# Kernel optimization log

Measured on AMD Instinct MI355X. Metric: run time of the kernel, lower is better.

Reference implementation:

```python
import jax, jax.numpy as jnp
import numpy as np

B, N, D, F, H, C, L = 64, 8192, 5, 16, 4, 4, 4
NEG_SLOPE = 0.2


def setup_inputs() -> dict:
    key = jax.random.key(0)
    ks = jax.random.split(key, 16)
    lin = lambda k, fi, fo: (jax.random.normal(k, (fi, fo), jnp.float32) / np.sqrt(fi)).astype(jnp.float32)
    x = jax.random.normal(ks[0], (B, N, F), jnp.float32)
    agent_nodes = jax.random.randint(ks[1], (B,), 0, N, dtype=jnp.int32)
    neighbors = jax.random.randint(ks[2], (N, D), 0, N, dtype=jnp.int32)
    # GATv2 params (L layers, all 16 -> 4 heads x 4 = 16)
    Wl = jax.random.normal(ks[3], (L, F, H, C), jnp.float32) / np.sqrt(F)
    Wr = jax.random.normal(ks[4], (L, F, H, C), jnp.float32) / np.sqrt(F)
    att_w = jax.random.normal(ks[5], (L, H, C), jnp.float32) / np.sqrt(C)
    bias = jnp.zeros((L, H * C), jnp.float32)
    # global classifier 16->32->64, edge classifier 99->16->8->1
    Wg1, bg1 = lin(ks[6], H * C, 2 * H * C), jnp.zeros(2 * H * C, jnp.float32)
    Wg2, bg2 = lin(ks[7], 2 * H * C, 4 * H * C), jnp.zeros(4 * H * C, jnp.float32)
    e_in = 2 * H * C + 3 + 4 * H * C  # 99
    We1, be1 = lin(ks[8], e_in, H * C), jnp.zeros(H * C, jnp.float32)
    We2, be2 = lin(ks[9], H * C, H * C // 2), jnp.zeros(H * C // 2, jnp.float32)
    We3, be3 = lin(ks[10], H * C // 2, 1), jnp.zeros(1, jnp.float32)
    return dict(x=x, agent_nodes=agent_nodes, neighbors=neighbors, Wl=Wl, Wr=Wr,
                att_w=att_w, bias=bias, Wg1=Wg1, bg1=bg1, Wg2=Wg2, bg2=bg2,
                We1=We1, be1=be1, We2=We2, be2=be2, We3=We3, be3=be3)


def _gatv2_layer(h, src, dst, wl, wr, a, b, n_nodes):
    # h: [B,N,Fin]; wl/wr: [Fin,H,C]; a: [H,C]; b: [H*C]
    xl = jnp.einsum('bnf,fhc->bnhc', h, wl)   # source transform
    xr = jnp.einsum('bnf,fhc->bnhc', h, wr)   # target transform
    hs = xl[:, src]                            # [B,E,H,C]
    ht = xr[:, dst]
    logit = jnp.einsum('behc,hc->beh', jax.nn.leaky_relu(hs + ht, NEG_SLOPE), a)
    lt = logit.transpose(1, 0, 2)              # [E,B,H] (segment ops need E first)
    m = jax.ops.segment_max(lt, dst, num_segments=n_nodes)
    w = jnp.exp(lt - m[dst])
    s = jax.ops.segment_sum(w, dst, num_segments=n_nodes)
    alpha = w / (s[dst] + 1e-16)               # [E,B,H] softmax over in-edges of dst
    msg = alpha[..., None] * hs.transpose(1, 0, 2, 3)
    out = jax.ops.segment_sum(msg, dst, num_segments=n_nodes)  # [N,B,H,C]
    return out.transpose(1, 0, 2, 3).reshape(h.shape[0], n_nodes, -1) + b


def reference(x, agent_nodes, neighbors, Wl, Wr, att_w, bias,
              Wg1, bg1, Wg2, bg2, We1, be1, We2, be2, We3, be3):
    Bn, Nn, _ = x.shape
    Dd = neighbors.shape[1]
    loop = jnp.arange(Nn, dtype=neighbors.dtype)
    src = jnp.concatenate([jnp.repeat(loop, Dd), loop])   # add_self_loops
    dst = jnp.concatenate([neighbors.reshape(-1), loop])
    h = x
    for i in range(Wl.shape[0]):
        h = _gatv2_layer(h, src, dst, Wl[i], Wr[i], att_w[i], bias[i], Nn)
    # global mean aggregation -> 2 SlimFC(tanh)
    agg = jnp.tanh(h.mean(axis=1) @ Wg1 + bg1)
    agg = jnp.tanh(agg @ Wg2 + bg2)                        # [B,64]
    # agent out-edges: source node + its D neighbors
    nb = neighbors[agent_nodes]                            # [B,D]
    bi = jnp.arange(Bn)
    source = h[bi, agent_nodes]                            # [B,16]
    target = h[bi[:, None], nb]                            # [B,D,16]
    tok = jnp.eye(3, dtype=h.dtype)                        # 3 one-hot act tokens
    feats = jnp.concatenate([
        jnp.broadcast_to(source[:, None, None, :], (Bn, 3, Dd, source.shape[-1])),
        jnp.broadcast_to(tok[None, :, None, :], (Bn, 3, Dd, 3)),
        jnp.broadcast_to(target[:, None, :, :], (Bn, 3, Dd, target.shape[-1])),
        jnp.broadcast_to(agg[:, None, None, :], (Bn, 3, Dd, agg.shape[-1])),
    ], axis=-1)                                            # [B,3,D,99]
    e = jnp.tanh(feats @ We1 + be1)
    e = jnp.tanh(e @ We2 + be2)
    e = (e @ We3 + be3)[..., 0]                            # [B,3,D]
    # logits[b, turn*D + move] (convert_multidiscrete_action_to_discrete)
    return e.reshape(Bn, 3 * Dd)
```

## Files before the change

kernel.cpp:

```cpp
#include <hip/hip_runtime.h>
#include <hip/hip_fp16.h>
#include <cmath>

#define NNODES 8192
#define NB 64
#define ND 5
#define MAXDEG 64
#define NBLK_T0 2048
#define NBLK_LAY 8192



__global__ void __launch_bounds__(256)
k_t0fill(const float* __restrict__ x, const float* __restrict__ Wl0, const float* __restrict__ Wr0,
         __half* __restrict__ xl0, __half* __restrict__ xr0,
         const int* __restrict__ agent, const int* __restrict__ nbr,
         int* __restrict__ cnt, int* __restrict__ slot, int* __restrict__ needed) {
  if (blockIdx.x >= NBLK_T0) {
    int eb = blockIdx.x - NBLK_T0;
    if (eb < 160) {
      int i = eb*256 + threadIdx.x;
      int v = nbr[i];
      int pos = atomicAdd(&cnt[v], 1);
      slot[v*MAXDEG + 1 + pos] = i/ND;
    } else if (threadIdx.x < NB) {
      int an = agent[threadIdx.x];
      needed[an] = 1;
      #pragma unroll
      for (int d = 0; d < ND; ++d) needed[nbr[an*ND + d]] = 1;
    }
    return;
  }
  int gid = blockIdx.x*blockDim.x + threadIdx.x;
  int n = gid >> 6;
  int b = gid & 63;
  const float4* src = (const float4*)(x + (((size_t)b*NNODES + n) << 4));
  float hv[16];
  #pragma unroll
  for (int q = 0; q < 4; ++q) *(float4*)(hv+4*q) = src[q];
  float yl[16], yr[16];
  #pragma unroll
  for (int j = 0; j < 16; ++j) { yl[j] = 0.f; yr[j] = 0.f; }
  #pragma unroll
  for (int f = 0; f < 16; ++f) {
    float hf = hv[f];
    #pragma unroll
    for (int j = 0; j < 16; ++j) {
      yl[j] = fmaf(hf, Wl0[f*16+j], yl[j]);
      yr[j] = fmaf(hf, Wr0[f*16+j], yr[j]);
    }
  }
  size_t idx = ((size_t)n << 10) + (b << 4);
  __half2 lh[8], rh[8];
  #pragma unroll
  for (int j = 0; j < 8; ++j) {
    lh[j] = __floats2half2_rn(yl[2*j], yl[2*j+1]);
    rh[j] = __floats2half2_rn(yr[2*j], yr[2*j+1]);
  }
  float4* ld = (float4*)(xl0 + idx);
  ld[0] = *(float4*)&lh[0]; ld[1] = *(float4*)&lh[4];
  float4* rd = (float4*)(xr0 + idx);
  rd[0] = *(float4*)&rh[0]; rd[1] = *(float4*)&rh[4];
}


template<bool LAST>
__global__ void __launch_bounds__(256)
k_layer(const __half* __restrict__ xlin, const __half* __restrict__ xrin,
        __half* __restrict__ xlout, __half* __restrict__ xrout,
        const float* __restrict__ WlNext, const float* __restrict__ WrNext,
        const float* __restrict__ att, const float* __restrict__ bias,
        const int* __restrict__ cnt, const int* __restrict__ slot,
        const int* __restrict__ needed, __half* __restrict__ h,
        float* __restrict__ meanpart) {
  __shared__ float sW[544];
  __shared__ float msm[4][16][17];
  int tid = threadIdx.x;
  int w = tid >> 6, lane = tid & 63;

  if (!LAST) {
    sW[tid]     = WlNext[tid];
    sW[256+tid] = WrNext[tid];
  }
  if (tid < 16)      sW[512+tid]    = att[tid];
  else if (tid < 32) sW[512+tid]    = bias[tid-16];
  __syncthreads();

  int wv = (blockIdx.x << 2) + w;
  int q = wv >> 13;
  int v = wv & (NNODES-1);
  int head = lane & 3;
  size_t soff = ((size_t)q << 8) + (lane << 2);

  float4 awv = *(float4*)&sW[512 + head*4];
  float aw0 = awv.x, aw1 = awv.y, aw2 = awv.z, aw3 = awv.w;

  float xr0, xr1, xr2, xr3;
  {
    float2 rx = *(const float2*)(xrin + (((size_t)v) << 10) + soff);
    __half2* ph = (__half2*)&rx;
    float2 f0 = __half22float2(ph[0]), f1 = __half22float2(ph[1]);
    xr0 = f0.x; xr1 = f0.y; xr2 = f1.x; xr3 = f1.y;
  }

  float s = 0.f, a0 = 0.f, a1 = 0.f, a2 = 0.f, a3 = 0.f;
  int deg = cnt[v];
  int tot = deg + 1;
  const int* sl = slot + v*MAXDEG;

  auto loadrow = [&](int u) -> float2 {
    return *(const float2*)(xlin + (((size_t)u) << 10) + soff);
  };
  auto process = [&](float2 r) {
    __half2* ph = (__half2*)&r;
    float2 f0 = __half22float2(ph[0]), f1 = __half22float2(ph[1]);
    float t0 = f0.x, t1 = f0.y, t2 = f1.x, t3 = f1.y;
    float z0 = t0 + xr0; z0 = (z0 >= 0.f) ? z0 : 0.2f*z0;
    float z1 = t1 + xr1; z1 = (z1 >= 0.f) ? z1 : 0.2f*z1;
    float z2 = t2 + xr2; z2 = (z2 >= 0.f) ? z2 : 0.2f*z2;
    float z3 = t3 + xr3; z3 = (z3 >= 0.f) ? z3 : 0.2f*z3;
    float lg = fmaf(z0, aw0, fmaf(z1, aw1, fmaf(z2, aw2, z3*aw3)));
    float p = __expf(lg);
    s += p;
    a0 = fmaf(p, t0, a0); a1 = fmaf(p, t1, a1);
    a2 = fmaf(p, t2, a2); a3 = fmaf(p, t3, a3);
  };

  float2 r0, r1, r2, r3, r4, r5, r6, r7, pA, pB;
  r0 = loadrow(v);
  if (tot > 1) r1 = loadrow(sl[1]);
  if (tot > 2) r2 = loadrow(sl[2]);
  if (tot > 3) r3 = loadrow(sl[3]);
  if (tot > 4) r4 = loadrow(sl[4]);
  if (tot > 5) r5 = loadrow(sl[5]);
  if (tot > 6) r6 = loadrow(sl[6]);
  if (tot > 7) r7 = loadrow(sl[7]);
  if (tot > 8) pA = loadrow(sl[8]);
  if (tot > 9) pB = loadrow(sl[9]);
  process(r0);
  if (tot > 1) process(r1);
  if (tot > 2) process(r2);
  if (tot > 3) process(r3);
  if (tot > 4) process(r4);
  if (tot > 5) process(r5);
  if (tot > 6) process(r6);
  if (tot > 7) process(r7);
  int e = 8;
  for (; e+1 < tot; e += 2) {
    float2 cA = pA; if (e+2 < tot) pA = loadrow(sl[e+2]);
    float2 cB = pB; if (e+3 < tot) pB = loadrow(sl[e+3]);
    process(cA); process(cB);
  }
  if (e < tot) process(pA);

  float inv = 1.f / s;
  float4 bsv = *(float4*)&sW[528 + head*4];
  float o0 = fmaf(a0, inv, bsv.x), o1 = fmaf(a1, inv, bsv.y);
  float o2 = fmaf(a2, inv, bsv.z), o3 = fmaf(a3, inv, bsv.w);

  if (!LAST) {
    float of[16];
    int lb = lane & ~3;
    #pragma unroll
    for (int src = 0; src < 4; ++src) {
      of[src*4+0] = __shfl(o0, lb+src);
      of[src*4+1] = __shfl(o1, lb+src);
      of[src*4+2] = __shfl(o2, lb+src);
      of[src*4+3] = __shfl(o3, lb+src);
    }
    float yl0=0.f, yl1=0.f, yl2=0.f, yl3=0.f;
    float yr0=0.f, yr1=0.f, yr2=0.f, yr3=0.f;
    #pragma unroll
    for (int f = 0; f < 16; ++f) {
      float4 wl4 = *(float4*)&sW[f*16 + head*4];
      float4 wr4 = *(float4*)&sW[256 + f*16 + head*4];
      float ofv = of[f];
      yl0 = fmaf(ofv, wl4.x, yl0); yl1 = fmaf(ofv, wl4.y, yl1);
      yl2 = fmaf(ofv, wl4.z, yl2); yl3 = fmaf(ofv, wl4.w, yl3);
      yr0 = fmaf(ofv, wr4.x, yr0); yr1 = fmaf(ofv, wr4.y, yr1);
      yr2 = fmaf(ofv, wr4.z, yr2); yr3 = fmaf(ofv, wr4.w, yr3);
    }
    float2 lo, ro;
    ((__half2*)&lo)[0] = __floats2half2_rn(yl0, yl1);
    ((__half2*)&lo)[1] = __floats2half2_rn(yl2, yl3);
    ((__half2*)&ro)[0] = __floats2half2_rn(yr0, yr1);
    ((__half2*)&ro)[1] = __floats2half2_rn(yr2, yr3);
    size_t idx = (((size_t)v) << 10) + soff;
    *(float2*)(xlout + idx) = lo;
    *(float2*)(xrout + idx) = ro;
  } else {
    if (needed[v]) {
      float2 ho;
      ((__half2*)&ho)[0] = __floats2half2_rn(o0, o1);
      ((__half2*)&ho)[1] = __floats2half2_rn(o2, o3);
      *(float2*)(h + (((size_t)v) << 10) + soff) = ho;
    }
    int bl = lane >> 2;
    msm[w][bl][head*4+0] = o0;
    msm[w][bl][head*4+1] = o1;
    msm[w][bl][head*4+2] = o2;
    msm[w][bl][head*4+3] = o3;
    __syncthreads();
    int bl2 = tid >> 4, hc = tid & 15;
    float ssum = msm[0][bl2][hc] + msm[1][bl2][hc] + msm[2][bl2][hc] + msm[3][bl2][hc];
    meanpart[(size_t)blockIdx.x*256 + tid] = ssum;
  }
}


__global__ void __launch_bounds__(256)
k_tail(const __half* __restrict__ h, const int* __restrict__ agent,
       const int* __restrict__ nbr, const float* __restrict__ meanpart,
       const float* __restrict__ Wg1, const float* __restrict__ bg1,
       const float* __restrict__ Wg2, const float* __restrict__ bg2,
       const float* __restrict__ We1, const float* __restrict__ be1,
       const float* __restrict__ We2, const float* __restrict__ be2,
       const float* __restrict__ We3, const float* __restrict__ be3,
       float* __restrict__ out) {
  int b = blockIdx.x;
  int t = threadIdx.x;
  __shared__ float red[256];
  __shared__ float mean[16], g1[32], aggs[64];
  __shared__ float srcv[16];
  __shared__ float tgt[5][16];
  __shared__ float e1s[15][16];
  __shared__ float e2s[15][8];
  int an = agent[b];

  {
    int hc = t & 15, grp = t >> 4;
    int q = b >> 4, bl = b & 15;
    float s = 0.f;
    int base = q*2048 + grp*128;
    for (int p = 0; p < 128; ++p)
      s += meanpart[(size_t)(base+p)*256 + bl*16 + hc];
    red[t] = s;
    __syncthreads();
    if (t < 16) {
      float m = 0.f;
      for (int g = 0; g < 16; ++g) m += red[g*16 + t];
      mean[t] = m * (1.0f/NNODES);
    }
  }
  if (t >= 64 && t < 80) srcv[t-64] = __half2float(h[((size_t)an << 10) + (b << 4) + (t-64)]);
  if (t >= 96 && t < 176) {
    int d = (t-96)/16, k = (t-96)%16;
    int nn = nbr[an*ND + d];
    tgt[d][k] = __half2float(h[((size_t)nn << 10) + (b << 4) + k]);
  }
  __syncthreads();
  if (t < 32) {
    float a = bg1[t];
    for (int f = 0; f < 16; ++f) a = fmaf(mean[f], Wg1[f*32+t], a);
    g1[t] = tanhf(a);
  }
  __syncthreads();
  if (t < 64) {
    float a = bg2[t];
    for (int f = 0; f < 32; ++f) a = fmaf(g1[f], Wg2[f*64+t], a);
    aggs[t] = tanhf(a);
  }
  __syncthreads();
  if (t < 240) {
    int j = t & 15, td = t >> 4;
    int tk = td/5, d = td%5;
    float a = be1[j];
    for (int k = 0; k < 16; ++k) a = fmaf(srcv[k],  We1[k*16+j],      a);
    a += We1[(16+tk)*16 + j];
    for (int k = 0; k < 16; ++k) a = fmaf(tgt[d][k], We1[(19+k)*16+j], a);
    for (int k = 0; k < 64; ++k) a = fmaf(aggs[k],  We1[(35+k)*16+j], a);
    e1s[td][j] = tanhf(a);
  }
  __syncthreads();
  if (t < 120) {
    int j = t & 7, td = t >> 3;
    float a = be2[j];
    for (int k = 0; k < 16; ++k) a = fmaf(e1s[td][k], We2[k*8+j], a);
    e2s[td][j] = tanhf(a);
  }
  __syncthreads();
  if (t < 15) {
    float a = be3[0];
    for (int k = 0; k < 8; ++k) a = fmaf(e2s[t][k], We3[k], a);
    out[b*15 + t] = a;
  }
}


extern "C" void kernel_launch(void* const* d_in, const int* in_sizes, int n_in,
                              void* d_out, int out_size, void* d_ws, size_t ws_size,
                              hipStream_t stream) {
  const float* x     = (const float*)d_in[0];
  const int*   agent = (const int*)  d_in[1];
  const int*   nbr   = (const int*)  d_in[2];
  const float* Wl    = (const float*)d_in[3];
  const float* Wr    = (const float*)d_in[4];
  const float* att   = (const float*)d_in[5];
  const float* bias  = (const float*)d_in[6];
  const float* Wg1   = (const float*)d_in[7];
  const float* bg1   = (const float*)d_in[8];
  const float* Wg2   = (const float*)d_in[9];
  const float* bg2   = (const float*)d_in[10];
  const float* We1   = (const float*)d_in[11];
  const float* be1   = (const float*)d_in[12];
  const float* We2   = (const float*)d_in[13];
  const float* be2   = (const float*)d_in[14];
  const float* We3   = (const float*)d_in[15];
  const float* be3   = (const float*)d_in[16];
  float* out = (float*)d_out;

  char* ws = (char*)d_ws;
  size_t off = 0;
  auto alloc = [&](size_t bytes) -> void* {
    void* p = ws + off;
    off += (bytes + 255) & ~(size_t)255;
    return p;
  };
  const size_t XBYTES = (size_t)NNODES*NB*16*sizeof(__half);
  __half* h    = (__half*)alloc(XBYTES);
  __half* xlA  = (__half*)alloc(XBYTES);
  __half* xlB  = (__half*)alloc(XBYTES);
  __half* xrA  = (__half*)alloc(XBYTES);
  __half* xrB  = (__half*)alloc(XBYTES);
  int*  slot   = (int*)alloc((size_t)NNODES*MAXDEG*sizeof(int));
  float* meanpart = (float*)alloc((size_t)NBLK_LAY*256*sizeof(float));
  int* cnt    = (int*)alloc(NNODES*sizeof(int));
  int* needed = (int*)alloc(NNODES*sizeof(int));

  hipMemsetAsync(cnt, 0, NNODES*sizeof(int)*2, stream);

  k_t0fill<<<NBLK_T0 + 161, 256, 0, stream>>>(x, Wl, Wr, xlA, xrA,
                                              agent, nbr, cnt, slot, needed);

  k_layer<false><<<NBLK_LAY, 256, 0, stream>>>(xlA, xrA, xlB, xrB, Wl + 256, Wr + 256,
                                               att,      bias,      cnt, slot, needed, nullptr, nullptr);
  k_layer<false><<<NBLK_LAY, 256, 0, stream>>>(xlB, xrB, xlA, xrA, Wl + 512, Wr + 512,
                                               att + 16, bias + 16, cnt, slot, needed, nullptr, nullptr);
  k_layer<false><<<NBLK_LAY, 256, 0, stream>>>(xlA, xrA, xlB, xrB, Wl + 768, Wr + 768,
                                               att + 32, bias + 32, cnt, slot, needed, nullptr, nullptr);
  k_layer<true ><<<NBLK_LAY, 256, 0, stream>>>(xlB, xrB, nullptr, nullptr, nullptr, nullptr,
                                               att + 48, bias + 48, cnt, slot, needed, h, meanpart);

  k_tail<<<NB, 256, 0, stream>>>(h, agent, nbr, meanpart,
                                 Wg1, bg1, Wg2, bg2,
                                 We1, be1, We2, be2, We3, be3, out);
}
```

Before: 238.1 us.

## Interleave batch quarters across blocks and use nontemporal loads and stores

Block-to-(node, batch-quarter) mapping is permuted so that consecutive blocks cover the four batch quarters of neighbouring node pairs, which is meant to improve L2 locality for the gathered neighbor rows that all quarters share. The xr load and the xl/xr/h/meanpart stores become nontemporal so streamed data does not evict the reused gathered rows from cache. The tail kernel's mean reduction is rewritten to follow the new block ordering. Nontemporal stores of data read by the next layer may lower its cache hit rate.

Measured after the change: 245.8 us. 1.03x slower.

```diff
diff --git a/kernel.cpp b/kernel.cpp
--- a/kernel.cpp
+++ b/kernel.cpp
@@ -9,6 +9,17 @@
 #define NBLK_T0 2048
 #define NBLK_LAY 8192
 
+
+__device__ __forceinline__ float2 nt_load_f2(const void* p) {
+  unsigned long long u = __builtin_nontemporal_load((const unsigned long long*)p);
+  return *(float2*)&u;
+}
+__device__ __forceinline__ void nt_store_f2(float2 v, void* p) {
+  __builtin_nontemporal_store(*(unsigned long long*)&v, (unsigned long long*)p);
+}
+__device__ __forceinline__ void nt_store_f(float v, void* p) {
+  __builtin_nontemporal_store(*(unsigned int*)&v, (unsigned int*)p);
+}
 
 
 __global__ void __launch_bounds__(256)
@@ -86,9 +97,9 @@
   else if (tid < 32) sW[512+tid]    = bias[tid-16];
   __syncthreads();
 
-  int wv = (blockIdx.x << 2) + w;
-  int q = wv >> 13;
-  int v = wv & (NNODES-1);
+  int B = blockIdx.x;
+  int q = (B >> 1) & 3;
+  int v = ((((B >> 3) << 1) | (B & 1)) << 2) + w;
   int head = lane & 3;
   size_t soff = ((size_t)q << 8) + (lane << 2);
 
@@ -97,7 +108,7 @@
 
   float xr0, xr1, xr2, xr3;
   {
-    float2 rx = *(const float2*)(xrin + (((size_t)v) << 10) + soff);
+    float2 rx = nt_load_f2(xrin + (((size_t)v) << 10) + soff);
     __half2* ph = (__half2*)&rx;
     float2 f0 = __half22float2(ph[0]), f1 = __half22float2(ph[1]);
     xr0 = f0.x; xr1 = f0.y; xr2 = f1.x; xr3 = f1.y;
@@ -186,14 +197,14 @@
     ((__half2*)&ro)[0] = __floats2half2_rn(yr0, yr1);
     ((__half2*)&ro)[1] = __floats2half2_rn(yr2, yr3);
     size_t idx = (((size_t)v) << 10) + soff;
-    *(float2*)(xlout + idx) = lo;
-    *(float2*)(xrout + idx) = ro;
+    nt_store_f2(lo, xlout + idx);
+    nt_store_f2(ro, xrout + idx);
   } else {
     if (needed[v]) {
       float2 ho;
       ((__half2*)&ho)[0] = __floats2half2_rn(o0, o1);
       ((__half2*)&ho)[1] = __floats2half2_rn(o2, o3);
-      *(float2*)(h + (((size_t)v) << 10) + soff) = ho;
+      nt_store_f2(ho, h + (((size_t)v) << 10) + soff);
     }
     int bl = lane >> 2;
     msm[w][bl][head*4+0] = o0;
@@ -203,7 +214,7 @@
     __syncthreads();
     int bl2 = tid >> 4, hc = tid & 15;
     float ssum = msm[0][bl2][hc] + msm[1][bl2][hc] + msm[2][bl2][hc] + msm[3][bl2][hc];
-    meanpart[(size_t)blockIdx.x*256 + tid] = ssum;
+    nt_store_f(ssum, meanpart + (size_t)B*256 + tid);
   }
 }
 
@@ -231,9 +242,11 @@
     int hc = t & 15, grp = t >> 4;
     int q = b >> 4, bl = b & 15;
     float s = 0.f;
-    int base = q*2048 + grp*128;
-    for (int p = 0; p < 128; ++p)
-      s += meanpart[(size_t)(base+p)*256 + bl*16 + hc];
+    for (int m = grp*64; m < grp*64+64; ++m) {
+      int B0 = (m << 3) | (q << 1);
+      s += meanpart[(size_t)B0*256 + bl*16 + hc]
+         + meanpart[(size_t)(B0|1)*256 + bl*16 + hc];
+    }
     red[t] = s;
     __syncthreads();
     if (t < 16) {
```
